# Optimization experiments

Hardware: AMD Instinct MI355X
Metric: run time of the kernel (lower is better)

The kernel has to match this reference:

```python
import jax, jax.numpy as jnp
import numpy as np

INIT_RANGE = 0.02


def setup_inputs() -> dict:
    key = jax.random.key(0)
    ks = jax.random.split(key, 7)
    B, S, E, H, D = 4, 2048, 1024, 16, 64
    return {
        "query": jax.random.normal(ks[0], (B, S, E), dtype=jnp.float32),
        "key": jax.random.normal(ks[1], (B, S, E), dtype=jnp.float32),
        "value": jax.random.normal(ks[2], (B, S, E), dtype=jnp.float32),
        "W_Q": jax.random.normal(ks[3], (H, E, D), dtype=jnp.float32) * INIT_RANGE,
        "W_K": jax.random.normal(ks[4], (H, E, D), dtype=jnp.float32) * INIT_RANGE,
        "W_V": jax.random.normal(ks[5], (H, E, D), dtype=jnp.float32) * INIT_RANGE,
        "W_O": jax.random.normal(ks[6], (H, D, E), dtype=jnp.float32) * INIT_RANGE,
        "b_Q": jnp.zeros((H, D), dtype=jnp.float32),
        "b_K": jnp.zeros((H, D), dtype=jnp.float32),
        "b_V": jnp.zeros((H, D), dtype=jnp.float32),
        "b_O": jnp.zeros((E,), dtype=jnp.float32),
    }


def reference(query, key, value, W_Q, W_K, W_V, W_O, b_Q, b_K, b_V, b_O):
    head_dim = W_Q.shape[-1]
    scale = 1.0 / jnp.sqrt(jnp.asarray(head_dim, dtype=query.dtype))
    # Per-head projections: [B,S,E] x [H,E,D] -> [B,S,H,D]
    Q = jnp.einsum('bse,hed->bshd', query, W_Q) + b_Q
    K = jnp.einsum('bse,hed->bshd', key, W_K) + b_K
    V = jnp.einsum('bse,hed->bshd', value, W_V) + b_V
    # Scores: [B,H,S_from,S_to]
    scores = jnp.einsum('bfhd,bthd->bhft', Q, K) * scale
    attn = jax.nn.softmax(scores, axis=-1)
    # Weighted values: [B,H,S,D]
    OV = jnp.einsum('bhft,bthd->bhfd', attn, V)
    # Output projection: [B,S,E]
    return jnp.einsum('bhsd,hde->bse', OV, W_O) + b_O
```

## Files before the change

kernel.cpp:

```cpp
#include <hip/hip_runtime.h>
#include <hip/hip_bf16.h>

typedef __attribute__((ext_vector_type(8))) short bf16x8;
typedef __attribute__((ext_vector_type(4))) float f32x4;
typedef __attribute__((ext_vector_type(16))) float f32x16;
typedef __attribute__((ext_vector_type(4))) int i32x4;

#define LOG2E 1.4426950408889634f

__device__ __forceinline__ short f2bf(float f){
  unsigned u = __float_as_uint(f);
  u += 0x7fffu + ((u >> 16) & 1u);
  return (short)(u >> 16);
}
__device__ __forceinline__ unsigned cvtpk(float lo, float hi){
  unsigned r;
  asm("v_cvt_pk_bf16_f32 %0, %1, %2" : "=v"(r) : "v"(lo), "v"(hi));
  return r;
}
__device__ __forceinline__ void plswap(unsigned &a, unsigned &b){
  asm("v_permlane32_swap_b32 %0, %1" : "+v"(a), "+v"(b));
}
__device__ __forceinline__ void gl_lds16(const short* g, short* l){
  __builtin_amdgcn_global_load_lds((const __attribute__((address_space(1))) void*)g,
                                   (__attribute__((address_space(3))) void*)l, 16, 0, 0);
}

__global__ __launch_bounds__(256) void prep_wqkv3(const float* __restrict__ Wq,
                                                  const float* __restrict__ Wk,
                                                  const float* __restrict__ Wv,
                                                  short* __restrict__ WqT,
                                                  short* __restrict__ WkT,
                                                  short* __restrict__ WvT){
  int idx = blockIdx.x * 256 + threadIdx.x;
  int e = idx & 1023, n = idx >> 10;
  int h = n >> 6, d = n & 63;
  int src = h * 65536 + e * 64 + d;
  WqT[idx] = f2bf(Wq[src]);
  WkT[idx] = f2bf(Wk[src]);
  WvT[idx] = f2bf(Wv[src]);
}
__global__ __launch_bounds__(256) void prep_wo(const float* __restrict__ W, short* __restrict__ Wt){
  int idx = blockIdx.x * 256 + threadIdx.x;
  int hd = idx & 1023, e = idx >> 10;
  Wt[idx] = f2bf(W[hd * 1024 + e]);
}
__global__ __launch_bounds__(256) void xconv3(const float* __restrict__ xq,
                                              const float* __restrict__ xk,
                                              const float* __restrict__ xv,
                                              short* __restrict__ oq,
                                              short* __restrict__ ok,
                                              short* __restrict__ ov){
  int idx = (blockIdx.x * 256 + threadIdx.x) * 8;
  #pragma unroll
  for (int a = 0; a < 3; ++a){
    const float* x = a == 0 ? xq : (a == 1 ? xk : xv);
    short* o = a == 0 ? oq : (a == 1 ? ok : ov);
    float4 v0 = *(const float4*)&x[idx];
    float4 v1 = *(const float4*)&x[idx + 4];
    bf16x8 t;
    t[0]=f2bf(v0.x); t[1]=f2bf(v0.y); t[2]=f2bf(v0.z); t[3]=f2bf(v0.w);
    t[4]=f2bf(v1.x); t[5]=f2bf(v1.y); t[6]=f2bf(v1.z); t[7]=f2bf(v1.w);
    *(bf16x8*)&o[idx] = t;
  }
}

__global__ __launch_bounds__(256) void proj_gemm(const short* __restrict__ A,
                                                 const short* __restrict__ Wt,
                                                 const float* __restrict__ bias,
                                                 short* __restrict__ Out,
                                                 float scale){
  __shared__ short Al[128][64];
  __shared__ short Bl[128][64];
  int tid = threadIdx.x;
  int bm0 = blockIdx.x * 128, bn0 = blockIdx.y * 128;
  int w = tid >> 6, lane = tid & 63;
  int wm = w >> 1, wn = w & 1;
  int r16 = lane & 15, kblk = lane >> 4;
  int srow = tid >> 3, schunk = tid & 7;

  f32x4 acc[4][4] = {};
  for (int kt = 0; kt < 16; ++kt){
    int k0 = kt * 64;
    __syncthreads();
    #pragma unroll
    for (int p = 0; p < 4; ++p){
      int row = p * 32 + srow;
      int sc = (schunk ^ (row & 7)) * 8;
      gl_lds16(A  + (size_t)(bm0 + row) * 1024 + k0 + sc, &Al[p * 32 + w * 8][0]);
      gl_lds16(Wt + (size_t)(bn0 + row) * 1024 + k0 + sc, &Bl[p * 32 + w * 8][0]);
    }
    __syncthreads();
    bf16x8 af[2][4], bfr[2][4];
    #pragma unroll
    for (int half = 0; half < 2; ++half){
      #pragma unroll
      for (int m = 0; m < 4; ++m){
        int r = wm * 64 + m * 16 + r16;
        af[half][m] = *(bf16x8*)&Al[r][(((half << 2) | kblk) ^ (r & 7)) * 8];
      }
      #pragma unroll
      for (int n = 0; n < 4; ++n){
        int r = wn * 64 + n * 16 + r16;
        bfr[half][n] = *(bf16x8*)&Bl[r][(((half << 2) | kblk) ^ (r & 7)) * 8];
      }
    }
    #pragma unroll
    for (int half = 0; half < 2; ++half)
      #pragma unroll
      for (int m = 0; m < 4; ++m)
        #pragma unroll
        for (int n = 0; n < 4; ++n)
          acc[m][n] = __builtin_amdgcn_mfma_f32_16x16x32_bf16(af[half][m], bfr[half][n], acc[m][n], 0, 0, 0);
  }
  #pragma unroll
  for (int m = 0; m < 4; ++m){
    int grow0 = bm0 + wm * 64 + m * 16 + kblk * 4;
    #pragma unroll
    for (int n = 0; n < 4; ++n){
      int gcol = bn0 + wn * 64 + n * 16 + r16;
      float bv = bias[gcol];
      int h = gcol >> 6, d = gcol & 63;
      #pragma unroll
      for (int i = 0; i < 4; ++i){
        int grow = grow0 + i;
        int b = grow >> 11, s = grow & 2047;
        Out[(size_t)((b * 16 + h) * 2048 + s) * 64 + d] = f2bf((acc[m][n][i] + bv) * scale);
      }
    }
  }
}

__global__ __launch_bounds__(256) void out_gemm(const short* __restrict__ A,
                                                const short* __restrict__ Wt,
                                                const float* __restrict__ bias,
                                                float* __restrict__ Out){
  __shared__ short Al[128][64];
  __shared__ short Bl[128][64];
  int tid = threadIdx.x;
  int bm0 = blockIdx.x * 128, bn0 = blockIdx.y * 128;
  int w = tid >> 6, lane = tid & 63;
  int wm = w >> 1, wn = w & 1;
  int r16 = lane & 15, kblk = lane >> 4;
  int srow = tid >> 3, schunk = tid & 7;
  f32x4 acc[4][4] = {};
  for (int kt = 0; kt < 16; ++kt){
    int k0 = kt * 64;
    __syncthreads();
    #pragma unroll
    for (int p = 0; p < 4; ++p){
      int row = p * 32 + srow;
      int sc = (schunk ^ (row & 7)) * 8;
      gl_lds16(A  + (size_t)(bm0 + row) * 1024 + k0 + sc, &Al[p * 32 + w * 8][0]);
      gl_lds16(Wt + (size_t)(bn0 + row) * 1024 + k0 + sc, &Bl[p * 32 + w * 8][0]);
    }
    __syncthreads();
    bf16x8 af[2][4], bfr[2][4];
    #pragma unroll
    for (int half = 0; half < 2; ++half){
      #pragma unroll
      for (int m = 0; m < 4; ++m){
        int r = wm * 64 + m * 16 + r16;
        af[half][m] = *(bf16x8*)&Al[r][(((half << 2) | kblk) ^ (r & 7)) * 8];
      }
      #pragma unroll
      for (int n = 0; n < 4; ++n){
        int r = wn * 64 + n * 16 + r16;
        bfr[half][n] = *(bf16x8*)&Bl[r][(((half << 2) | kblk) ^ (r & 7)) * 8];
      }
    }
    #pragma unroll
    for (int half = 0; half < 2; ++half)
      #pragma unroll
      for (int m = 0; m < 4; ++m)
        #pragma unroll
        for (int n = 0; n < 4; ++n)
          acc[m][n] = __builtin_amdgcn_mfma_f32_16x16x32_bf16(af[half][m], bfr[half][n], acc[m][n], 0, 0, 0);
  }
  #pragma unroll
  for (int m = 0; m < 4; ++m){
    int grow0 = bm0 + wm * 64 + m * 16 + kblk * 4;
    #pragma unroll
    for (int n = 0; n < 4; ++n){
      int gcol = bn0 + wn * 64 + n * 16 + r16;
      float bv = bias[gcol];
      #pragma unroll
      for (int i = 0; i < 4; ++i)
        Out[(size_t)(grow0 + i) * 1024 + gcol] = acc[m][n][i] + bv;
    }
  }
}

__global__ __launch_bounds__(256) void vtrans(const short* __restrict__ V, short* __restrict__ Vt){
  __shared__ short t[64][68];
  int bh = blockIdx.x >> 5, ts = blockIdx.x & 31;
  int tid = threadIdx.x;
  int r = tid >> 4, c4 = (tid & 15) * 4;
  const short* src = V + ((size_t)bh * 2048 + ts * 64) * 64;
  #pragma unroll
  for (int p = 0; p < 4; ++p){
    int row = p * 16 + r;
    *(short4*)&t[row][c4] = *(const short4*)&src[row * 64 + c4];
  }
  __syncthreads();
  short* dst = Vt + (size_t)bh * 64 * 2048 + ts * 64;
  #pragma unroll
  for (int p = 0; p < 4; ++p){
    int d = p * 16 + r;
    short4 o = make_short4(t[c4 + 0][d], t[c4 + 1][d], t[c4 + 2][d], t[c4 + 3][d]);
    *(short4*)&dst[(size_t)d * 2048 + c4] = o;
  }
}

__device__ __forceinline__ f32x16 mfma32(bf16x8 a, bf16x8 b, f32x16 c){
  return __builtin_amdgcn_mfma_f32_32x32x16_bf16(a, b, c, 0, 0, 0);
}

#define ATT_BODY(T, CUR, NXT)                                                          \
  {                                                                                    \
    if ((T) + 1 < 32){                                                                 \
      _Pragma("unroll")                                                                \
      for (int p = 0; p < 2; ++p){                                                     \
        int row = p * 32 + srow;                                                       \
        gl_lds16(Kp + (size_t)(((T) + 1) * 64 + row) * 64 + sx, &Kl[NXT][p * 32 + w * 8][0]); \
        gl_lds16(Vp + (size_t)row * 2048 + ((T) + 1) * 64 + sx, &Vl[NXT][p * 32 + w * 8][0]); \
      }                                                                                \
    }                                                                                  \
    f32x16 s0 = {}, s1 = {};                                                           \
    _Pragma("unroll")                                                                  \
    for (int c = 0; c < 4; ++c){                                                       \
      bf16x8 kf0 = *(const bf16x8*)&Kl[CUR][l31][rchunk[c]];                           \
      bf16x8 kf1 = *(const bf16x8*)&Kl[CUR][32 + l31][rchunk[c]];                      \
      s0 = mfma32(kf0, qf[c], s0);                                                     \
      s1 = mfma32(kf1, qf[c], s1);                                                     \
    }                                                                                  \
    _Pragma("unroll")                                                                  \
    for (int r = 0; r < 16; ++r) s0[r] = __builtin_amdgcn_exp2f(s0[r]);                \
    _Pragma("unroll")                                                                  \
    for (int r = 0; r < 16; ++r) s1[r] = __builtin_amdgcn_exp2f(s1[r]);                \
    float u8_[8];                                                                      \
    _Pragma("unroll")                                                                  \
    for (int r = 0; r < 8; ++r)                                                        \
      u8_[r] = (s0[r] + s0[r + 8]) + (s1[r] + s1[r + 8]);                              \
    float rs = ((u8_[0] + u8_[1]) + (u8_[2] + u8_[3])) + ((u8_[4] + u8_[5]) + (u8_[6] + u8_[7])); \
    rs += __shfl_xor(rs, 32);                                                          \
    lrow += rs;                                                                        \
    bf16x8 pb[4];                                                                      \
    _Pragma("unroll")                                                                  \
    for (int cc = 0; cc < 2; ++cc){                                                    \
      int b0 = cc * 8;                                                                 \
      unsigned u0 = cvtpk(s0[b0 + 0], s0[b0 + 1]);                                     \
      unsigned u1 = cvtpk(s0[b0 + 2], s0[b0 + 3]);                                     \
      unsigned w0 = cvtpk(s0[b0 + 4], s0[b0 + 5]);                                     \
      unsigned w1 = cvtpk(s0[b0 + 6], s0[b0 + 7]);                                     \
      plswap(u0, w0); plswap(u1, w1);                                                  \
      i32x4 pk0; pk0[0] = (int)u0; pk0[1] = (int)u1; pk0[2] = (int)w0; pk0[3] = (int)w1; \
      pb[cc] = __builtin_bit_cast(bf16x8, pk0);                                        \
      unsigned y0 = cvtpk(s1[b0 + 0], s1[b0 + 1]);                                     \
      unsigned y1 = cvtpk(s1[b0 + 2], s1[b0 + 3]);                                     \
      unsigned z0 = cvtpk(s1[b0 + 4], s1[b0 + 5]);                                     \
      unsigned z1 = cvtpk(s1[b0 + 6], s1[b0 + 7]);                                     \
      plswap(y0, z0); plswap(y1, z1);                                                  \
      i32x4 pk1; pk1[0] = (int)y0; pk1[1] = (int)y1; pk1[2] = (int)z0; pk1[3] = (int)z1; \
      pb[2 + cc] = __builtin_bit_cast(bf16x8, pk1);                                    \
    }                                                                                  \
    _Pragma("unroll")                                                                  \
    for (int c = 0; c < 4; ++c){                                                       \
      bf16x8 vf0 = *(const bf16x8*)&Vl[CUR][l31][rchunk[c]];                           \
      bf16x8 vf1 = *(const bf16x8*)&Vl[CUR][32 + l31][rchunk[c]];                      \
      acc0 = mfma32(vf0, pb[c], acc0);                                                 \
      acc1 = mfma32(vf1, pb[c], acc1);                                                 \
    }                                                                                  \
    __syncthreads();                                                                   \
  }

__global__ __launch_bounds__(256, 4) void attn(const short* __restrict__ Qb,
                                               const short* __restrict__ Kb,
                                               const short* __restrict__ Vtb,
                                               short* __restrict__ OVb){
  __shared__ short Kl[2][64][64];
  __shared__ short Vl[2][64][64];
  int tid = threadIdx.x;
  int w = tid >> 6, lane = tid & 63;
  int l31 = lane & 31, hi = lane >> 5;
  int bh = blockIdx.x & 63, qb = blockIdx.x >> 6;
  const short* Qp = Qb + ((size_t)bh * 2048 + qb * 128 + w * 32) * 64;
  const short* Kp = Kb + (size_t)bh * 2048 * 64;
  const short* Vp = Vtb + (size_t)bh * 64 * 2048;
  int srow = tid >> 3, schunk = tid & 7;
  int sx = (schunk ^ (srow & 7)) * 8;

  int rchunk[4];
  #pragma unroll
  for (int c = 0; c < 4; ++c) rchunk[c] = (((c << 1) | hi) ^ (l31 & 7)) * 8;

  #pragma unroll
  for (int p = 0; p < 2; ++p){
    int row = p * 32 + srow;
    gl_lds16(Kp + (size_t)row * 64 + sx, &Kl[0][p * 32 + w * 8][0]);
    gl_lds16(Vp + (size_t)row * 2048 + sx, &Vl[0][p * 32 + w * 8][0]);
  }

  bf16x8 qf[4];
  #pragma unroll
  for (int c = 0; c < 4; ++c)
    qf[c] = *(const bf16x8*)&Qp[l31 * 64 + c * 16 + hi * 8];

  f32x16 acc0 = {}, acc1 = {};
  float lrow = 0.f;
  __syncthreads();

  for (int t = 0; t < 32; t += 2){
    ATT_BODY(t, 0, 1)
    ATT_BODY(t + 1, 1, 0)
  }

  int b = bh >> 4, h = bh & 15;
  float inv = 1.0f / lrow;
  int q = qb * 128 + w * 32 + l31;
  size_t base = ((size_t)(b * 2048 + q)) * 1024 + h * 64;
  #pragma unroll
  for (int rg = 0; rg < 4; ++rg){
    short4 o0 = make_short4(f2bf(acc0[rg * 4 + 0] * inv),
                            f2bf(acc0[rg * 4 + 1] * inv),
                            f2bf(acc0[rg * 4 + 2] * inv),
                            f2bf(acc0[rg * 4 + 3] * inv));
    *(short4*)&OVb[base + rg * 8 + hi * 4] = o0;
    short4 o1 = make_short4(f2bf(acc1[rg * 4 + 0] * inv),
                            f2bf(acc1[rg * 4 + 1] * inv),
                            f2bf(acc1[rg * 4 + 2] * inv),
                            f2bf(acc1[rg * 4 + 3] * inv));
    *(short4*)&OVb[base + 32 + rg * 8 + hi * 4] = o1;
  }
}

extern "C" void kernel_launch(void* const* d_in, const int* in_sizes, int n_in,
                              void* d_out, int out_size, void* d_ws, size_t ws_size,
                              hipStream_t stream) {
  const float* query = (const float*)d_in[0];
  const float* key_  = (const float*)d_in[1];
  const float* value = (const float*)d_in[2];
  const float* W_Q = (const float*)d_in[3];
  const float* W_K = (const float*)d_in[4];
  const float* W_V = (const float*)d_in[5];
  const float* W_O = (const float*)d_in[6];
  const float* b_Q = (const float*)d_in[7];
  const float* b_K = (const float*)d_in[8];
  const float* b_V = (const float*)d_in[9];
  const float* b_O = (const float*)d_in[10];

  char* ws = (char*)d_ws;
  const size_t MB2 = 2097152, MB16 = 16777216;
  short* WqT = (short*)(ws + 0);
  short* WkT = (short*)(ws + MB2);
  short* WvT = (short*)(ws + 2 * MB2);
  short* WoT = (short*)(ws + 3 * MB2);
  short* RA = (short*)(ws + 4 * MB2);
  short* RB = (short*)(ws + 4 * MB2 + MB16);
  short* RC = (short*)(ws + 4 * MB2 + 2 * MB16);
  short* RD = (short*)(ws + 4 * MB2 + 3 * MB16);
  short* Xq = RA, *Xk = RB, *Xv = RC;
  short* Qb = RD;
  short* Kb = RA;
  short* Vb = RB;
  short* Vtb = RC;
  short* OVb = RB;

  prep_wqkv3<<<4096, 256, 0, stream>>>(W_Q, W_K, W_V, WqT, WkT, WvT);
  prep_wo  <<<4096, 256, 0, stream>>>(W_O, WoT);
  xconv3   <<<4096, 256, 0, stream>>>(query, key_, value, Xq, Xk, Xv);

  dim3 g(64, 8);
  proj_gemm<<<g, 256, 0, stream>>>(Xq, WqT, b_Q, Qb, LOG2E * 0.125f);
  proj_gemm<<<g, 256, 0, stream>>>(Xk, WkT, b_K, Kb, 1.0f);
  proj_gemm<<<g, 256, 0, stream>>>(Xv, WvT, b_V, Vb, 1.0f);

  vtrans<<<2048, 256, 0, stream>>>(Vb, Vtb);

  attn<<<1024, 256, 0, stream>>>(Qb, Kb, Vtb, OVb);

  out_gemm<<<g, 256, 0, stream>>>(OVb, WoT, b_O, (float*)d_out);
}
```

Measured before the change: 231.4 us.

## Double query rows per attention wave and tile weight-transpose prep kernels

The attention kernel now has each wave handle 64 query rows, as two 32-row groups, instead of 32. Each K/V fragment loaded from LDS then feeds twice as many MFMAs. The grid halves to 512 blocks and launch bounds drop to 2 blocks per CU to make room for the doubled accumulators and Q fragments. Separately, the weight-transpose prep kernels now use a 64x64 LDS tile with vectorized float4 loads and 16-byte stores instead of scattered per-element accesses. The trade-offs are higher register pressure, reduced occupancy, and fewer blocks to spread across CUs.

```diff
diff --git a/kernel.cpp b/kernel.cpp
--- a/kernel.cpp
+++ b/kernel.cpp
@@ -32,18 +32,52 @@
                                                   short* __restrict__ WqT,
                                                   short* __restrict__ WkT,
                                                   short* __restrict__ WvT){
-  int idx = blockIdx.x * 256 + threadIdx.x;
-  int e = idx & 1023, n = idx >> 10;
-  int h = n >> 6, d = n & 63;
-  int src = h * 65536 + e * 64 + d;
-  WqT[idx] = f2bf(Wq[src]);
-  WkT[idx] = f2bf(Wk[src]);
-  WvT[idx] = f2bf(Wv[src]);
+  __shared__ short t[64][72];
+  int h = blockIdx.x >> 4, et = blockIdx.x & 15;
+  int tid = threadIdx.x;
+  int er = tid >> 2, qc = (tid & 3) * 16;
+  #pragma unroll
+  for (int a = 0; a < 3; ++a){
+    const float* W = a == 0 ? Wq : (a == 1 ? Wk : Wv);
+    short* Wt = a == 0 ? WqT : (a == 1 ? WkT : WvT);
+    if (a) __syncthreads();
+    const float* src = W + h * 65536 + (et * 64 + er) * 64 + qc;
+    #pragma unroll
+    for (int v = 0; v < 4; ++v){
+      float4 f = *(const float4*)(src + v * 4);
+      t[qc + v * 4 + 0][er] = f2bf(f.x);
+      t[qc + v * 4 + 1][er] = f2bf(f.y);
+      t[qc + v * 4 + 2][er] = f2bf(f.z);
+      t[qc + v * 4 + 3][er] = f2bf(f.w);
+    }
+    __syncthreads();
+    bf16x8 o0 = *(const bf16x8*)&t[er][qc];
+    bf16x8 o1 = *(const bf16x8*)&t[er][qc + 8];
+    size_t dst = (size_t)(h * 64 + er) * 1024 + et * 64 + qc;
+    *(bf16x8*)&Wt[dst] = o0;
+    *(bf16x8*)&Wt[dst + 8] = o1;
+  }
 }
 __global__ __launch_bounds__(256) void prep_wo(const float* __restrict__ W, short* __restrict__ Wt){
-  int idx = blockIdx.x * 256 + threadIdx.x;
-  int hd = idx & 1023, e = idx >> 10;
-  Wt[idx] = f2bf(W[hd * 1024 + e]);
+  __shared__ short t[64][72];
+  int bi = blockIdx.x >> 4, bj = blockIdx.x & 15;
+  int tid = threadIdx.x;
+  int r = tid >> 2, qc = (tid & 3) * 16;
+  const float* src = W + (size_t)(bi * 64 + r) * 1024 + bj * 64 + qc;
+  #pragma unroll
+  for (int v = 0; v < 4; ++v){
+    float4 f = *(const float4*)(src + v * 4);
+    t[qc + v * 4 + 0][r] = f2bf(f.x);
+    t[qc + v * 4 + 1][r] = f2bf(f.y);
+    t[qc + v * 4 + 2][r] = f2bf(f.z);
+    t[qc + v * 4 + 3][r] = f2bf(f.w);
+  }
+  __syncthreads();
+  bf16x8 o0 = *(const bf16x8*)&t[r][qc];
+  bf16x8 o1 = *(const bf16x8*)&t[r][qc + 8];
+  size_t dst = (size_t)(bj * 64 + r) * 1024 + bi * 64 + qc;
+  *(bf16x8*)&Wt[dst] = o0;
+  *(bf16x8*)&Wt[dst + 8] = o1;
 }
 __global__ __launch_bounds__(256) void xconv3(const float* __restrict__ xq,
                                               const float* __restrict__ xk,
@@ -214,6 +248,38 @@
 
 __device__ __forceinline__ f32x16 mfma32(bf16x8 a, bf16x8 b, f32x16 c){
   return __builtin_amdgcn_mfma_f32_32x32x16_bf16(a, b, c, 0, 0, 0);
+}
+
+__device__ __forceinline__ void sm_pack(f32x16& s0, f32x16& s1, float& lrow, bf16x8* pb){
+  #pragma unroll
+  for (int r = 0; r < 16; ++r) s0[r] = __builtin_amdgcn_exp2f(s0[r]);
+  #pragma unroll
+  for (int r = 0; r < 16; ++r) s1[r] = __builtin_amdgcn_exp2f(s1[r]);
+  float u8_[8];
+  #pragma unroll
+  for (int r = 0; r < 8; ++r)
+    u8_[r] = (s0[r] + s0[r + 8]) + (s1[r] + s1[r + 8]);
+  float rs = ((u8_[0] + u8_[1]) + (u8_[2] + u8_[3])) + ((u8_[4] + u8_[5]) + (u8_[6] + u8_[7]));
+  rs += __shfl_xor(rs, 32);
+  lrow += rs;
+  #pragma unroll
+  for (int cc = 0; cc < 2; ++cc){
+    int b0 = cc * 8;
+    unsigned u0 = cvtpk(s0[b0 + 0], s0[b0 + 1]);
+    unsigned u1 = cvtpk(s0[b0 + 2], s0[b0 + 3]);
+    unsigned w0 = cvtpk(s0[b0 + 4], s0[b0 + 5]);
+    unsigned w1 = cvtpk(s0[b0 + 6], s0[b0 + 7]);
+    plswap(u0, w0); plswap(u1, w1);
+    i32x4 pk0; pk0[0] = (int)u0; pk0[1] = (int)u1; pk0[2] = (int)w0; pk0[3] = (int)w1;
+    pb[cc] = __builtin_bit_cast(bf16x8, pk0);
+    unsigned y0 = cvtpk(s1[b0 + 0], s1[b0 + 1]);
+    unsigned y1 = cvtpk(s1[b0 + 2], s1[b0 + 3]);
+    unsigned z0 = cvtpk(s1[b0 + 4], s1[b0 + 5]);
+    unsigned z1 = cvtpk(s1[b0 + 6], s1[b0 + 7]);
+    plswap(y0, z0); plswap(y1, z1);
+    i32x4 pk1; pk1[0] = (int)y0; pk1[1] = (int)y1; pk1[2] = (int)z0; pk1[3] = (int)z1;
+    pb[2 + cc] = __builtin_bit_cast(bf16x8, pk1);
+  }
 }
 
 #define ATT_BODY(T, CUR, NXT)                                                          \
@@ -226,55 +292,32 @@
         gl_lds16(Vp + (size_t)row * 2048 + ((T) + 1) * 64 + sx, &Vl[NXT][p * 32 + w * 8][0]); \
       }                                                                                \
     }                                                                                  \
-    f32x16 s0 = {}, s1 = {};                                                           \
+    f32x16 sA0 = {}, sA1 = {}, sB0 = {}, sB1 = {};                                     \
     _Pragma("unroll")                                                                  \
     for (int c = 0; c < 4; ++c){                                                       \
       bf16x8 kf0 = *(const bf16x8*)&Kl[CUR][l31][rchunk[c]];                           \
       bf16x8 kf1 = *(const bf16x8*)&Kl[CUR][32 + l31][rchunk[c]];                      \
-      s0 = mfma32(kf0, qf[c], s0);                                                     \
-      s1 = mfma32(kf1, qf[c], s1);                                                     \
+      sA0 = mfma32(kf0, qfA[c], sA0);                                                  \
+      sA1 = mfma32(kf1, qfA[c], sA1);                                                  \
+      sB0 = mfma32(kf0, qfB[c], sB0);                                                  \
+      sB1 = mfma32(kf1, qfB[c], sB1);                                                  \
     }                                                                                  \
-    _Pragma("unroll")                                                                  \
-    for (int r = 0; r < 16; ++r) s0[r] = __builtin_amdgcn_exp2f(s0[r]);                \
-    _Pragma("unroll")                                                                  \
-    for (int r = 0; r < 16; ++r) s1[r] = __builtin_amdgcn_exp2f(s1[r]);                \
-    float u8_[8];                                                                      \
-    _Pragma("unroll")                                                                  \
-    for (int r = 0; r < 8; ++r)                                                        \
-      u8_[r] = (s0[r] + s0[r + 8]) + (s1[r] + s1[r + 8]);                              \
-    float rs = ((u8_[0] + u8_[1]) + (u8_[2] + u8_[3])) + ((u8_[4] + u8_[5]) + (u8_[6] + u8_[7])); \
-    rs += __shfl_xor(rs, 32);                                                          \
-    lrow += rs;                                                                        \
-    bf16x8 pb[4];                                                                      \
-    _Pragma("unroll")                                                                  \
-    for (int cc = 0; cc < 2; ++cc){                                                    \
-      int b0 = cc * 8;                                                                 \
-      unsigned u0 = cvtpk(s0[b0 + 0], s0[b0 + 1]);                                     \
-      unsigned u1 = cvtpk(s0[b0 + 2], s0[b0 + 3]);                                     \
-      unsigned w0 = cvtpk(s0[b0 + 4], s0[b0 + 5]);                                     \
-      unsigned w1 = cvtpk(s0[b0 + 6], s0[b0 + 7]);                                     \
-      plswap(u0, w0); plswap(u1, w1);                                                  \
-      i32x4 pk0; pk0[0] = (int)u0; pk0[1] = (int)u1; pk0[2] = (int)w0; pk0[3] = (int)w1; \
-      pb[cc] = __builtin_bit_cast(bf16x8, pk0);                                        \
-      unsigned y0 = cvtpk(s1[b0 + 0], s1[b0 + 1]);                                     \
-      unsigned y1 = cvtpk(s1[b0 + 2], s1[b0 + 3]);                                     \
-      unsigned z0 = cvtpk(s1[b0 + 4], s1[b0 + 5]);                                     \
-      unsigned z1 = cvtpk(s1[b0 + 6], s1[b0 + 7]);                                     \
-      plswap(y0, z0); plswap(y1, z1);                                                  \
-      i32x4 pk1; pk1[0] = (int)y0; pk1[1] = (int)y1; pk1[2] = (int)z0; pk1[3] = (int)z1; \
-      pb[2 + cc] = __builtin_bit_cast(bf16x8, pk1);                                    \
-    }                                                                                  \
+    bf16x8 pbA[4], pbB[4];                                                             \
+    sm_pack(sA0, sA1, lrowA, pbA);                                                     \
+    sm_pack(sB0, sB1, lrowB, pbB);                                                     \
     _Pragma("unroll")                                                                  \
     for (int c = 0; c < 4; ++c){                                                       \
       bf16x8 vf0 = *(const bf16x8*)&Vl[CUR][l31][rchunk[c]];                           \
       bf16x8 vf1 = *(const bf16x8*)&Vl[CUR][32 + l31][rchunk[c]];                      \
-      acc0 = mfma32(vf0, pb[c], acc0);                                                 \
-      acc1 = mfma32(vf1, pb[c], acc1);                                                 \
+      accA0 = mfma32(vf0, pbA[c], accA0);                                              \
+      accA1 = mfma32(vf1, pbA[c], accA1);                                              \
+      accB0 = mfma32(vf0, pbB[c], accB0);                                              \
+      accB1 = mfma32(vf1, pbB[c], accB1);                                              \
     }                                                                                  \
     __syncthreads();                                                                   \
   }
 
-__global__ __launch_bounds__(256, 4) void attn(const short* __restrict__ Qb,
+__global__ __launch_bounds__(256, 2) void attn(const short* __restrict__ Qb,
                                                const short* __restrict__ Kb,
                                                const short* __restrict__ Vtb,
                                                short* __restrict__ OVb){
@@ -284,7 +327,7 @@
   int w = tid >> 6, lane = tid & 63;
   int l31 = lane & 31, hi = lane >> 5;
   int bh = blockIdx.x & 63, qb = blockIdx.x >> 6;
-  const short* Qp = Qb + ((size_t)bh * 2048 + qb * 128 + w * 32) * 64;
+  const short* Qp = Qb + ((size_t)bh * 2048 + qb * 256 + w * 64) * 64;
   const short* Kp = Kb + (size_t)bh * 2048 * 64;
   const short* Vp = Vtb + (size_t)bh * 64 * 2048;
   int srow = tid >> 3, schunk = tid & 7;
@@ -301,13 +344,15 @@
     gl_lds16(Vp + (size_t)row * 2048 + sx, &Vl[0][p * 32 + w * 8][0]);
   }
 
-  bf16x8 qf[4];
-  #pragma unroll
-  for (int c = 0; c < 4; ++c)
-    qf[c] = *(const bf16x8*)&Qp[l31 * 64 + c * 16 + hi * 8];
-
-  f32x16 acc0 = {}, acc1 = {};
-  float lrow = 0.f;
+  bf16x8 qfA[4], qfB[4];
+  #pragma unroll
+  for (int c = 0; c < 4; ++c){
+    qfA[c] = *(const bf16x8*)&Qp[l31 * 64 + c * 16 + hi * 8];
+    qfB[c] = *(const bf16x8*)&Qp[(32 + l31) * 64 + c * 16 + hi * 8];
+  }
+
+  f32x16 accA0 = {}, accA1 = {}, accB0 = {}, accB1 = {};
+  float lrowA = 0.f, lrowB = 0.f;
   __syncthreads();
 
   for (int t = 0; t < 32; t += 2){
@@ -316,21 +361,25 @@
   }
 
   int b = bh >> 4, h = bh & 15;
-  float inv = 1.0f / lrow;
-  int q = qb * 128 + w * 32 + l31;
-  size_t base = ((size_t)(b * 2048 + q)) * 1024 + h * 64;
+  int q0 = qb * 256 + w * 64 + l31;
+  float invA = 1.0f / lrowA;
+  float invB = 1.0f / lrowB;
+  size_t baseA = ((size_t)(b * 2048 + q0)) * 1024 + h * 64;
+  size_t baseB = baseA + (size_t)32 * 1024;
   #pragma unroll
   for (int rg = 0; rg < 4; ++rg){
-    short4 o0 = make_short4(f2bf(acc0[rg * 4 + 0] * inv),
-                            f2bf(acc0[rg * 4 + 1] * inv),
-                            f2bf(acc0[rg * 4 + 2] * inv),
-                            f2bf(acc0[rg * 4 + 3] * inv));
-    *(short4*)&OVb[base + rg * 8 + hi * 4] = o0;
-    short4 o1 = make_short4(f2bf(acc1[rg * 4 + 0] * inv),
-                            f2bf(acc1[rg * 4 + 1] * inv),
-                            f2bf(acc1[rg * 4 + 2] * inv),
-                            f2bf(acc1[rg * 4 + 3] * inv));
-    *(short4*)&OVb[base + 32 + rg * 8 + hi * 4] = o1;
+    short4 a0 = make_short4(f2bf(accA0[rg * 4 + 0] * invA), f2bf(accA0[rg * 4 + 1] * invA),
+                            f2bf(accA0[rg * 4 + 2] * invA), f2bf(accA0[rg * 4 + 3] * invA));
+    *(short4*)&OVb[baseA + rg * 8 + hi * 4] = a0;
+    short4 a1 = make_short4(f2bf(accA1[rg * 4 + 0] * invA), f2bf(accA1[rg * 4 + 1] * invA),
+                            f2bf(accA1[rg * 4 + 2] * invA), f2bf(accA1[rg * 4 + 3] * invA));
+    *(short4*)&OVb[baseA + 32 + rg * 8 + hi * 4] = a1;
+    short4 b0 = make_short4(f2bf(accB0[rg * 4 + 0] * invB), f2bf(accB0[rg * 4 + 1] * invB),
+                            f2bf(accB0[rg * 4 + 2] * invB), f2bf(accB0[rg * 4 + 3] * invB));
+    *(short4*)&OVb[baseB + rg * 8 + hi * 4] = b0;
+    short4 b1 = make_short4(f2bf(accB1[rg * 4 + 0] * invB), f2bf(accB1[rg * 4 + 1] * invB),
+                            f2bf(accB1[rg * 4 + 2] * invB), f2bf(accB1[rg * 4 + 3] * invB));
+    *(short4*)&OVb[baseB + 32 + rg * 8 + hi * 4] = b1;
   }
 }
 
@@ -366,8 +415,8 @@
   short* Vtb = RC;
   short* OVb = RB;
 
-  prep_wqkv3<<<4096, 256, 0, stream>>>(W_Q, W_K, W_V, WqT, WkT, WvT);
-  prep_wo  <<<4096, 256, 0, stream>>>(W_O, WoT);
+  prep_wqkv3<<<256, 256, 0, stream>>>(W_Q, W_K, W_V, WqT, WkT, WvT);
+  prep_wo  <<<256, 256, 0, stream>>>(W_O, WoT);
   xconv3   <<<4096, 256, 0, stream>>>(query, key_, value, Xq, Xk, Xv);
 
   dim3 g(64, 8);
@@ -377,7 +426,7 @@
 
   vtrans<<<2048, 256, 0, stream>>>(Vb, Vtb);
 
-  attn<<<1024, 256, 0, stream>>>(Qb, Kb, Vtb, OVb);
+  attn<<<512, 256, 0, stream>>>(Qb, Kb, Vtb, OVb);
 
   out_gemm<<<g, 256, 0, stream>>>(OVb, WoT, b_O, (float*)d_out);
 }
```

Measured after the change: 214.3 us. 1.08x faster.
